# Kernel tuning notes

Hardware: AMD Instinct MI355X
Metric: run time of the kernel (lower is better)

The kernel has to match this reference:

```python
import jax, jax.numpy as jnp
import numpy as np

B, E, D, H, A = 65536, 16, 256, 64, 18  # batch, n_subpolicies, emb_dim, hidden, n_actions


def setup_inputs() -> dict:
    key = jax.random.key(0)
    ks = jax.random.split(key, 16)
    s = lambda k, sh: jax.random.normal(k, sh, dtype=jnp.float32) * 0.05
    return dict(
        obs=s(ks[0], (B, D)),
        h=s(ks[1], (B, D)),
        c=s(ks[2], (B, D)),
        idxs=jax.random.randint(ks[3], (B,), 0, E, dtype=jnp.int32),
        # Observer: LSTMCell(D, D) params (torch layout: [4D, D] with i,f,g,o gate order)
        W_ih=s(ks[4], (4 * D, D)), W_hh=s(ks[5], (4 * D, D)),
        b_ih=s(ks[6], (4 * D,)), b_hh=s(ks[7], (4 * D,)),
        # Stacked SubPolicy actor params: Linear(D,64)-Tanh-Linear(64,A)
        Wa1=s(ks[8], (E, D, H)), ba1=s(ks[9], (E, H)),
        Wa2=s(ks[10], (E, H, A)), ba2=s(ks[11], (E, A)),
        # Stacked SubPolicy critic params: Linear(D,64)-Tanh-Linear(64,1)
        Wc1=s(ks[12], (E, D, H)), bc1=s(ks[13], (E, H)),
        Wc2=s(ks[14], (E, H, 1)), bc2=s(ks[15], (E, 1)),
    )


def reference(obs, h, c, idxs, W_ih, W_hh, b_ih, b_hh,
              Wa1, ba1, Wa2, ba2, Wc1, bc1, Wc2, bc2):
    # ---- Observer: single LSTMCell step ----
    gates = obs @ W_ih.T + b_ih + h @ W_hh.T + b_hh          # [B, 4D]
    gi, gf, gg, go = jnp.split(gates, 4, axis=1)
    i = jax.nn.sigmoid(gi); f = jax.nn.sigmoid(gf); o = jax.nn.sigmoid(go)
    c_new = f * c + i * jnp.tanh(gg)                          # [B, D]
    h_new = o * jnp.tanh(c_new)                               # [B, D]

    # ---- Expert dispatch: evaluate all tiny subpolicy MLPs, select per sample ----
    # (mathematically identical to the per-sample routing loop in forward_sub)
    ha = jnp.tanh(jnp.einsum('bd,edh->beh', h_new, Wa1) + ba1)        # [B, E, H]
    logits_all = jnp.einsum('beh,eha->bea', ha, Wa2) + ba2            # [B, E, A]
    hc = jnp.tanh(jnp.einsum('bd,edh->beh', h_new, Wc1) + bc1)        # [B, E, H]
    vals_all = (jnp.einsum('beh,eho->beo', hc, Wc2) + bc2)[..., 0]    # [B, E]

    b = jnp.arange(h_new.shape[0])
    logits = logits_all[b, idxs]                                       # [B, A]
    values = vals_all[b, idxs]                                         # [B]
    return (h_new, c_new, logits, values)
```

## Files before the change

kernel.cpp:

```cpp
#include <hip/hip_runtime.h>
#include <hip/hip_bf16.h>
#include <math.h>

#define NB 65536
#define ND 256
#define NE 16
#define NH 64
#define NA 18

typedef __bf16 bf16;
typedef __bf16 bf16x4 __attribute__((ext_vector_type(4)));
typedef __bf16 bf16x8 __attribute__((ext_vector_type(8)));
typedef float  f32x4  __attribute__((ext_vector_type(4)));

#define OFF_WCAT 0u
#define OFF_BCAT 1048576u
#define OFF_PW1  1052672u
#define OFF_B1   2101248u
#define OFF_CUR  2109440u
#define OFF_PERM 2109504u

__device__ __forceinline__ float sigm_(float x) {
    return 1.f / (1.f + __expf(-x));
}
__device__ __forceinline__ float tanh_(float x) {
    float cl = fminf(fmaxf(x, -15.f), 15.f);
    float e = __expf(2.f * cl);
    return (e - 1.f) / (e + 1.f);
}

__global__ void k_prep1(const float* __restrict__ W_ih, const float* __restrict__ W_hh,
                        const float* __restrict__ b_ih, const float* __restrict__ b_hh,
                        char* __restrict__ ws) {
    int t = blockIdx.x * 256 + threadIdx.x;
    bf16* Wcat = (bf16*)(ws + OFF_WCAT);
    int kc = t & 63, col = t >> 6;
    int k = kc * 8;
    const float* src = (k < 256) ? (W_ih + (size_t)col * 256 + k)
                                 : (W_hh + (size_t)col * 256 + (k - 256));
    float4 v0 = *(const float4*)(src);
    float4 v1 = *(const float4*)(src + 4);
    bf16x8 o;
    o[0] = (bf16)v0.x; o[1] = (bf16)v0.y; o[2] = (bf16)v0.z; o[3] = (bf16)v0.w;
    o[4] = (bf16)v1.x; o[5] = (bf16)v1.y; o[6] = (bf16)v1.z; o[7] = (bf16)v1.w;
    *(bf16x8*)(Wcat + ((size_t)kc * 1024 + col) * 8) = o;
    if (t < 1024) ((float*)(ws + OFF_BCAT))[t] = b_ih[t] + b_hh[t];
    if (t < 16)   ((int*)(ws + OFF_CUR))[t] = t * 65536;
}

__global__ void k_prep2(const float* __restrict__ Wa1, const float* __restrict__ Wc1,
                        const float* __restrict__ ba1, const float* __restrict__ bc1,
                        char* __restrict__ ws) {
    int t = blockIdx.x * 256 + threadIdx.x;
    bf16* PW1 = (bf16*)(ws + OFF_PW1);
    int col = t & 127, kc = (t >> 7) & 31, e = t >> 12;
    bf16x8 o;
#pragma unroll
    for (int j = 0; j < 8; ++j) {
        int k = kc * 8 + j;
        float v = (col < 64) ? Wa1[((size_t)e * 256 + k) * 64 + col]
                             : Wc1[((size_t)e * 256 + k) * 64 + (col - 64)];
        o[j] = (bf16)v;
    }
    *(bf16x8*)(PW1 + (((size_t)e * 32 + kc) * 128 + col) * 8) = o;
    if (t < 2048) {
        int e2 = t >> 7, c = t & 127;
        ((float*)(ws + OFF_B1))[t] = (c < 64) ? ba1[e2 * 64 + c] : bc1[e2 * 64 + (c - 64)];
    }
}

__global__ void k_scatter(const int* __restrict__ idxs, char* __restrict__ ws) {
    __shared__ int lh[16], lbase[16];
    int t = threadIdx.x;
    int i = blockIdx.x * 256 + t;
    if (t < 16) lh[t] = 0;
    __syncthreads();
    int e = idxs[i];
    int r = atomicAdd(&lh[e], 1);
    __syncthreads();
    int* cur = (int*)(ws + OFF_CUR);
    if (t < 16) lbase[t] = atomicAdd(&cur[t], lh[t]);
    __syncthreads();
    ((int*)(ws + OFF_PERM))[lbase[e] + r] = i;
}

__global__ __launch_bounds__(512, 4) void k_lstm(
    const float* __restrict__ obs, const float* __restrict__ hin,
    const float* __restrict__ cin, const float* __restrict__ bcat,
    const bf16* __restrict__ Wcat,
    float* __restrict__ hout, float* __restrict__ cout) {
    __shared__ alignas(16) char Asmem[2][8192];
    const int tid  = threadIdx.x;
    const int wave = tid >> 6, lane = tid & 63;
    const int lr = lane & 15, lk = lane >> 4;
    const int rb = blockIdx.x & 1023, chalf = blockIdx.x >> 10;
    const int row0 = rb * 64;
    const int srow = tid >> 3, sf = tid & 7;
    const int colc = chalf * 128 + wave * 16 + lr;

    const int wbyte = sf * 1024 + ((srow ^ sf) * 16);
    int rbo[2][4];
#pragma unroll
    for (int kf = 0; kf < 2; ++kf)
#pragma unroll
        for (int m = 0; m < 4; ++m) {
            int kc = kf * 4 + lk, R = m * 16 + lr;
            rbo[kf][m] = kc * 1024 + ((R ^ kc) * 16);
        }

    const float* pObs = obs + (size_t)(row0 + srow) * 256 + sf * 8;
    const float* pH   = hin + (size_t)(row0 + srow) * 256 + sf * 8;
    const bf16*  pB   = Wcat + ((size_t)lk * 1024 + colc) * 8;

    f32x4 acc[4][4];
#pragma unroll
    for (int m = 0; m < 4; ++m)
#pragma unroll
        for (int g = 0; g < 4; ++g)
#pragma unroll
            for (int r = 0; r < 4; ++r) acc[m][g][r] = 0.f;

    {
        float4 v0 = *(const float4*)pObs;
        float4 v1 = *(const float4*)(pObs + 4);
        bf16x8 o;
        o[0] = (bf16)v0.x; o[1] = (bf16)v0.y; o[2] = (bf16)v0.z; o[3] = (bf16)v0.w;
        o[4] = (bf16)v1.x; o[5] = (bf16)v1.y; o[6] = (bf16)v1.z; o[7] = (bf16)v1.w;
        *(bf16x8*)(&Asmem[0][wbyte]) = o;
    }
    __syncthreads();

#pragma unroll
    for (int ks = 0; ks < 8; ++ks) {
        const int cur = ks & 1;
        float4 n0, n1;
        if (ks < 7) {
            const float* sp = (ks < 3) ? (pObs + (ks + 1) * 64) : (pH + (ks - 3) * 64);
            n0 = *(const float4*)sp;
            n1 = *(const float4*)(sp + 4);
        }
        const char* Ab = Asmem[cur];
#pragma unroll
        for (int kf = 0; kf < 2; ++kf) {
            bf16x8 a[4];
#pragma unroll
            for (int m = 0; m < 4; ++m)
                a[m] = *(const bf16x8*)(Ab + rbo[kf][m]);
            const bf16* pBk = pB + (size_t)(ks * 8 + kf * 4) * 1024 * 8;
            bf16x8 b0 = *(const bf16x8*)(pBk);
            bf16x8 b1 = *(const bf16x8*)(pBk + 256 * 8);
            bf16x8 b2 = *(const bf16x8*)(pBk + 512 * 8);
            bf16x8 b3 = *(const bf16x8*)(pBk + 768 * 8);
#pragma unroll
            for (int m = 0; m < 4; ++m) {
                acc[m][0] = __builtin_amdgcn_mfma_f32_16x16x32_bf16(a[m], b0, acc[m][0], 0, 0, 0);
                acc[m][1] = __builtin_amdgcn_mfma_f32_16x16x32_bf16(a[m], b1, acc[m][1], 0, 0, 0);
                acc[m][2] = __builtin_amdgcn_mfma_f32_16x16x32_bf16(a[m], b2, acc[m][2], 0, 0, 0);
                acc[m][3] = __builtin_amdgcn_mfma_f32_16x16x32_bf16(a[m], b3, acc[m][3], 0, 0, 0);
            }
        }
        if (ks < 7) {
            bf16x8 o;
            o[0] = (bf16)n0.x; o[1] = (bf16)n0.y; o[2] = (bf16)n0.z; o[3] = (bf16)n0.w;
            o[4] = (bf16)n1.x; o[5] = (bf16)n1.y; o[6] = (bf16)n1.z; o[7] = (bf16)n1.w;
            *(bf16x8*)(&Asmem[cur ^ 1][wbyte]) = o;
            __syncthreads();
        }
    }

    float bi = bcat[colc], bf_ = bcat[256 + colc], bg = bcat[512 + colc], bo = bcat[768 + colc];
#pragma unroll
    for (int m = 0; m < 4; ++m) {
#pragma unroll
        for (int r = 0; r < 4; ++r) {
            int row = row0 + m * 16 + lk * 4 + r;
            float gi = acc[m][0][r] + bi;
            float gf = acc[m][1][r] + bf_;
            float gg = acc[m][2][r] + bg;
            float go = acc[m][3][r] + bo;
            float iv = sigm_(gi), fv = sigm_(gf), gv = tanh_(gg), ov = sigm_(go);
            float co = cin[(size_t)row * 256 + colc];
            float cn = fv * co + iv * gv;
            float hn = ov * tanh_(cn);
            cout[(size_t)row * 256 + colc] = cn;
            hout[(size_t)row * 256 + colc] = hn;
        }
    }
}

__global__ __launch_bounds__(256) void k_expert(
    const float* __restrict__ Wa2, const float* __restrict__ ba2,
    const float* __restrict__ Wc2, const float* __restrict__ bc2,
    char* __restrict__ ws, const float* __restrict__ hsrc,
    float* __restrict__ lout, float* __restrict__ vout) {
    const int e = blockIdx.y;
    const int* cur = (const int*)(ws + OFF_CUR);
    int cnt = cur[e] - e * 65536;
    int r0 = blockIdx.x * 64;
    if (r0 >= cnt) return;
    int nr = min(64, cnt - r0);
    const int* permE = (const int*)(ws + OFF_PERM) + (size_t)e * 65536 + r0;

    __shared__ int rows_s[64];
    __shared__ alignas(16) char smem[128 * 66 * 4];
    bf16*  Alds = (bf16*)smem;
    float* haF  = (float*)smem;

    int t = threadIdx.x;
    if (t < 64) rows_s[t] = permE[(t < nr) ? t : 0];
    __syncthreads();

    {
        int rowi = t >> 2, q = t & 3;
        const float* hp = hsrc + (size_t)rows_s[rowi] * 256;
#pragma unroll
        for (int s = 0; s < 8; ++s) {
            int kc = s * 4 + q;
            float4 v0 = *(const float4*)(hp + kc * 8);
            float4 v1 = *(const float4*)(hp + kc * 8 + 4);
            bf16x8 o;
            o[0] = (bf16)v0.x; o[1] = (bf16)v0.y; o[2] = (bf16)v0.z; o[3] = (bf16)v0.w;
            o[4] = (bf16)v1.x; o[5] = (bf16)v1.y; o[6] = (bf16)v1.z; o[7] = (bf16)v1.w;
            *(bf16x8*)(Alds + ((size_t)kc * 64 + rowi) * 8) = o;
        }
    }
    __syncthreads();

    const bf16* PW1 = (const bf16*)(ws + OFF_PW1) + (size_t)e * 32 * 128 * 8;
    const float* b1 = (const float*)(ws + OFF_B1) + e * 128;
    int wave = t >> 6, lane = t & 63, lr = lane & 15, lk = lane >> 4;

    f32x4 acc[4][2];
#pragma unroll
    for (int m = 0; m < 4; ++m)
#pragma unroll
        for (int n = 0; n < 2; ++n)
#pragma unroll
            for (int r = 0; r < 4; ++r) acc[m][n][r] = 0.f;

#pragma unroll
    for (int kf = 0; kf < 8; ++kf) {
        bf16x8 a[4], bb[2];
#pragma unroll
        for (int m = 0; m < 4; ++m)
            a[m] = *(const bf16x8*)(Alds + (((kf * 4 + lk) * 64) + (m * 16 + lr)) * 8);
#pragma unroll
        for (int n = 0; n < 2; ++n) {
            int colh = wave * 32 + n * 16 + lr;
            int kc = kf * 4 + lk;
            bb[n] = *(const bf16x8*)(PW1 + ((size_t)kc * 128 + colh) * 8);
        }
#pragma unroll
        for (int m = 0; m < 4; ++m)
#pragma unroll
            for (int n = 0; n < 2; ++n)
                acc[m][n] = __builtin_amdgcn_mfma_f32_16x16x32_bf16(a[m], bb[n], acc[m][n], 0, 0, 0);
    }
    __syncthreads();

#pragma unroll
    for (int m = 0; m < 4; ++m)
#pragma unroll
        for (int n = 0; n < 2; ++n) {
            int colh = wave * 32 + n * 16 + lr;
            float bbv = b1[colh];
#pragma unroll
            for (int r = 0; r < 4; ++r) {
                int row = m * 16 + lk * 4 + r;
                haF[colh * 66 + row] = tanh_(acc[m][n][r] + bbv);
            }
        }
    __syncthreads();

    int row = t & 63;
    int grow = rows_s[row];
    bool valid = row < nr;
#pragma unroll
    for (int p = 0; p < 5; ++p) {
        int aI = p * 4 + (t >> 6);
        if (aI < NA) {
            float s = ba2[e * NA + aI];
            for (int hh = 0; hh < 64; ++hh)
                s += haF[hh * 66 + row] * Wa2[((size_t)e * 64 + hh) * NA + aI];
            if (valid) lout[(size_t)grow * NA + aI] = s;
        }
    }
    if (t < 64) {
        float s = bc2[e];
        for (int hh = 0; hh < 64; ++hh)
            s += haF[(64 + hh) * 66 + row] * Wc2[e * 64 + hh];
        if (valid) vout[grow] = s;
    }
}

extern "C" void kernel_launch(void* const* d_in, const int* in_sizes, int n_in,
                              void* d_out, int out_size, void* d_ws, size_t ws_size,
                              hipStream_t stream) {
    const float* obs  = (const float*)d_in[0];
    const float* h    = (const float*)d_in[1];
    const float* c    = (const float*)d_in[2];
    const int*   idxs = (const int*)d_in[3];
    const float* W_ih = (const float*)d_in[4];
    const float* W_hh = (const float*)d_in[5];
    const float* b_ih = (const float*)d_in[6];
    const float* b_hh = (const float*)d_in[7];
    const float* Wa1  = (const float*)d_in[8];
    const float* ba1  = (const float*)d_in[9];
    const float* Wa2  = (const float*)d_in[10];
    const float* ba2  = (const float*)d_in[11];
    const float* Wc1  = (const float*)d_in[12];
    const float* bc1  = (const float*)d_in[13];
    const float* Wc2  = (const float*)d_in[14];
    const float* bc2  = (const float*)d_in[15];

    float* out  = (float*)d_out;
    float* hout = out;
    float* cout = out + (size_t)NB * ND;
    float* lout = out + (size_t)2 * NB * ND;
    float* vout = lout + (size_t)NB * NA;
    char* ws = (char*)d_ws;

    k_prep1<<<dim3(256), dim3(256), 0, stream>>>(W_ih, W_hh, b_ih, b_hh, ws);
    k_prep2<<<dim3(256), dim3(256), 0, stream>>>(Wa1, Wc1, ba1, bc1, ws);
    k_scatter<<<dim3(256), dim3(256), 0, stream>>>(idxs, ws);
    k_lstm<<<dim3(2048), dim3(512), 0, stream>>>(
        obs, h, c, (const float*)(ws + OFF_BCAT), (const bf16*)(ws + OFF_WCAT), hout, cout);
    k_expert<<<dim3(1024, 16), dim3(256), 0, stream>>>(
        Wa2, ba2, Wc2, bc2, ws, hout, lout, vout);
}
```

Before: 193.9 us.

## Stage full A tile in LDS up front and use fast reciprocal in activations

The LSTM GEMM kernel used to double-buffer 8 KB slices of the obs/h tile with a barrier per k-step. It now loads and converts the whole 64x512 bf16 A tile into 64 KB of LDS in one pass, syncs once, then runs a barrier-free 16-step MFMA loop. This issues all global loads at once and drops the per-step barriers, but the larger LDS footprint may cut how many blocks fit per CU (launch bounds ask for 4). Sigmoid and tanh also swap the divide for the hardware rcp instruction, which is slightly less precise.

After: 211.2 us. 1.09x slower.

```diff
diff --git a/kernel.cpp b/kernel.cpp
--- a/kernel.cpp
+++ b/kernel.cpp
@@ -20,13 +20,14 @@
 #define OFF_CUR  2109440u
 #define OFF_PERM 2109504u
 
+__device__ __forceinline__ float rcp_(float x) { return __builtin_amdgcn_rcpf(x); }
 __device__ __forceinline__ float sigm_(float x) {
-    return 1.f / (1.f + __expf(-x));
+    return rcp_(1.f + __expf(-x));
 }
 __device__ __forceinline__ float tanh_(float x) {
     float cl = fminf(fmaxf(x, -15.f), 15.f);
     float e = __expf(2.f * cl);
-    return (e - 1.f) / (e + 1.f);
+    return (e - 1.f) * rcp_(e + 1.f);
 }
 
 __global__ void k_prep1(const float* __restrict__ W_ih, const float* __restrict__ W_hh,
@@ -89,28 +90,39 @@
     const float* __restrict__ cin, const float* __restrict__ bcat,
     const bf16* __restrict__ Wcat,
     float* __restrict__ hout, float* __restrict__ cout) {
-    __shared__ alignas(16) char Asmem[2][8192];
+    __shared__ alignas(16) char Alds[65536];
     const int tid  = threadIdx.x;
     const int wave = tid >> 6, lane = tid & 63;
     const int lr = lane & 15, lk = lane >> 4;
     const int rb = blockIdx.x & 1023, chalf = blockIdx.x >> 10;
     const int row0 = rb * 64;
-    const int srow = tid >> 3, sf = tid & 7;
     const int colc = chalf * 128 + wave * 16 + lr;
 
-    const int wbyte = sf * 1024 + ((srow ^ sf) * 16);
-    int rbo[2][4];
-#pragma unroll
-    for (int kf = 0; kf < 2; ++kf)
-#pragma unroll
-        for (int m = 0; m < 4; ++m) {
-            int kc = kf * 4 + lk, R = m * 16 + lr;
-            rbo[kf][m] = kc * 1024 + ((R ^ kc) * 16);
-        }
-
-    const float* pObs = obs + (size_t)(row0 + srow) * 256 + sf * 8;
-    const float* pH   = hin + (size_t)(row0 + srow) * 256 + sf * 8;
-    const bf16*  pB   = Wcat + ((size_t)lk * 1024 + colc) * 8;
+    {
+        int sr = tid >> 3, j = tid & 7;
+        const float* baseO = obs + (size_t)(row0 + sr) * 256;
+        const float* baseH = hin + (size_t)(row0 + sr) * 256;
+#pragma unroll
+        for (int s = 0; s < 8; ++s) {
+            int kc = s * 8 + j;
+            const float* sp = (s < 4) ? (baseO + kc * 8) : (baseH + (kc - 32) * 8);
+            float4 v0 = *(const float4*)sp;
+            float4 v1 = *(const float4*)(sp + 4);
+            bf16x8 o;
+            o[0] = (bf16)v0.x; o[1] = (bf16)v0.y; o[2] = (bf16)v0.z; o[3] = (bf16)v0.w;
+            o[4] = (bf16)v1.x; o[5] = (bf16)v1.y; o[6] = (bf16)v1.z; o[7] = (bf16)v1.w;
+            *(bf16x8*)(Alds + kc * 1024 + (((sr ^ (kc & 7))) * 16)) = o;
+        }
+    }
+    __syncthreads();
+
+    int offE[4], offO[4];
+#pragma unroll
+    for (int m = 0; m < 4; ++m) {
+        int R = m * 16 + lr;
+        offE[m] = lk * 1024 + ((R ^ lk) * 16);
+        offO[m] = lk * 1024 + ((R ^ (lk + 4)) * 16);
+    }
 
     f32x4 acc[4][4];
 #pragma unroll
@@ -120,52 +132,44 @@
 #pragma unroll
             for (int r = 0; r < 4; ++r) acc[m][g][r] = 0.f;
 
-    {
-        float4 v0 = *(const float4*)pObs;
-        float4 v1 = *(const float4*)(pObs + 4);
-        bf16x8 o;
-        o[0] = (bf16)v0.x; o[1] = (bf16)v0.y; o[2] = (bf16)v0.z; o[3] = (bf16)v0.w;
-        o[4] = (bf16)v1.x; o[5] = (bf16)v1.y; o[6] = (bf16)v1.z; o[7] = (bf16)v1.w;
-        *(bf16x8*)(&Asmem[0][wbyte]) = o;
-    }
-    __syncthreads();
-
-#pragma unroll
-    for (int ks = 0; ks < 8; ++ks) {
-        const int cur = ks & 1;
-        float4 n0, n1;
-        if (ks < 7) {
-            const float* sp = (ks < 3) ? (pObs + (ks + 1) * 64) : (pH + (ks - 3) * 64);
-            n0 = *(const float4*)sp;
-            n1 = *(const float4*)(sp + 4);
-        }
-        const char* Ab = Asmem[cur];
-#pragma unroll
-        for (int kf = 0; kf < 2; ++kf) {
-            bf16x8 a[4];
-#pragma unroll
-            for (int m = 0; m < 4; ++m)
-                a[m] = *(const bf16x8*)(Ab + rbo[kf][m]);
-            const bf16* pBk = pB + (size_t)(ks * 8 + kf * 4) * 1024 * 8;
-            bf16x8 b0 = *(const bf16x8*)(pBk);
-            bf16x8 b1 = *(const bf16x8*)(pBk + 256 * 8);
-            bf16x8 b2 = *(const bf16x8*)(pBk + 512 * 8);
-            bf16x8 b3 = *(const bf16x8*)(pBk + 768 * 8);
-#pragma unroll
-            for (int m = 0; m < 4; ++m) {
-                acc[m][0] = __builtin_amdgcn_mfma_f32_16x16x32_bf16(a[m], b0, acc[m][0], 0, 0, 0);
-                acc[m][1] = __builtin_amdgcn_mfma_f32_16x16x32_bf16(a[m], b1, acc[m][1], 0, 0, 0);
-                acc[m][2] = __builtin_amdgcn_mfma_f32_16x16x32_bf16(a[m], b2, acc[m][2], 0, 0, 0);
-                acc[m][3] = __builtin_amdgcn_mfma_f32_16x16x32_bf16(a[m], b3, acc[m][3], 0, 0, 0);
-            }
-        }
-        if (ks < 7) {
-            bf16x8 o;
-            o[0] = (bf16)n0.x; o[1] = (bf16)n0.y; o[2] = (bf16)n0.z; o[3] = (bf16)n0.w;
-            o[4] = (bf16)n1.x; o[5] = (bf16)n1.y; o[6] = (bf16)n1.z; o[7] = (bf16)n1.w;
-            *(bf16x8*)(&Asmem[cur ^ 1][wbyte]) = o;
-            __syncthreads();
-        }
+    const bf16* pB = Wcat + ((size_t)lk * 1024 + colc) * 8;
+
+#pragma unroll
+    for (int kf = 0; kf < 16; ++kf) {
+        const char* Ab = Alds + kf * 4096;
+        bf16x8 a0, a1, a2, a3;
+        if (kf & 1) {
+            a0 = *(const bf16x8*)(Ab + offO[0]);
+            a1 = *(const bf16x8*)(Ab + offO[1]);
+            a2 = *(const bf16x8*)(Ab + offO[2]);
+            a3 = *(const bf16x8*)(Ab + offO[3]);
+        } else {
+            a0 = *(const bf16x8*)(Ab + offE[0]);
+            a1 = *(const bf16x8*)(Ab + offE[1]);
+            a2 = *(const bf16x8*)(Ab + offE[2]);
+            a3 = *(const bf16x8*)(Ab + offE[3]);
+        }
+        const bf16* pBk = pB + (size_t)kf * 4 * 1024 * 8;
+        bf16x8 b0 = *(const bf16x8*)(pBk);
+        bf16x8 b1 = *(const bf16x8*)(pBk + 256 * 8);
+        bf16x8 b2 = *(const bf16x8*)(pBk + 512 * 8);
+        bf16x8 b3 = *(const bf16x8*)(pBk + 768 * 8);
+        acc[0][0] = __builtin_amdgcn_mfma_f32_16x16x32_bf16(a0, b0, acc[0][0], 0, 0, 0);
+        acc[0][1] = __builtin_amdgcn_mfma_f32_16x16x32_bf16(a0, b1, acc[0][1], 0, 0, 0);
+        acc[0][2] = __builtin_amdgcn_mfma_f32_16x16x32_bf16(a0, b2, acc[0][2], 0, 0, 0);
+        acc[0][3] = __builtin_amdgcn_mfma_f32_16x16x32_bf16(a0, b3, acc[0][3], 0, 0, 0);
+        acc[1][0] = __builtin_amdgcn_mfma_f32_16x16x32_bf16(a1, b0, acc[1][0], 0, 0, 0);
+        acc[1][1] = __builtin_amdgcn_mfma_f32_16x16x32_bf16(a1, b1, acc[1][1], 0, 0, 0);
+        acc[1][2] = __builtin_amdgcn_mfma_f32_16x16x32_bf16(a1, b2, acc[1][2], 0, 0, 0);
+        acc[1][3] = __builtin_amdgcn_mfma_f32_16x16x32_bf16(a1, b3, acc[1][3], 0, 0, 0);
+        acc[2][0] = __builtin_amdgcn_mfma_f32_16x16x32_bf16(a2, b0, acc[2][0], 0, 0, 0);
+        acc[2][1] = __builtin_amdgcn_mfma_f32_16x16x32_bf16(a2, b1, acc[2][1], 0, 0, 0);
+        acc[2][2] = __builtin_amdgcn_mfma_f32_16x16x32_bf16(a2, b2, acc[2][2], 0, 0, 0);
+        acc[2][3] = __builtin_amdgcn_mfma_f32_16x16x32_bf16(a2, b3, acc[2][3], 0, 0, 0);
+        acc[3][0] = __builtin_amdgcn_mfma_f32_16x16x32_bf16(a3, b0, acc[3][0], 0, 0, 0);
+        acc[3][1] = __builtin_amdgcn_mfma_f32_16x16x32_bf16(a3, b1, acc[3][1], 0, 0, 0);
+        acc[3][2] = __builtin_amdgcn_mfma_f32_16x16x32_bf16(a3, b2, acc[3][2], 0, 0, 0);
+        acc[3][3] = __builtin_amdgcn_mfma_f32_16x16x32_bf16(a3, b3, acc[3][3], 0, 0, 0);
     }
 
     float bi = bcat[colc], bf_ = bcat[256 + colc], bg = bcat[512 + colc], bo = bcat[768 + colc];
```
